# Performance work log

Hardware: AMD Instinct MI355X
Metric: run time of the kernel (lower is better)

## Reference

```python
import jax, jax.numpy as jnp
import numpy as np

K_NEIGHBOURS = 40  # includes self; self is dropped after top-k


def setup_inputs() -> dict:
    key = jax.random.key(0)
    ks = jax.random.split(key, 4)
    B, V, F_in = 4, 4096, 64
    P, S, F_out = 64, 4, 64
    x = jax.random.normal(ks[0], (B, V, F_in), dtype=jnp.float32)
    Wf = jax.random.normal(ks[1], (F_in, P), dtype=jnp.float32) / np.sqrt(F_in)
    bf = jnp.zeros((P,), dtype=jnp.float32)
    Ws = jax.random.normal(ks[2], (F_in, S), dtype=jnp.float32) / np.sqrt(F_in)
    bs = jnp.zeros((S,), dtype=jnp.float32)
    Wo = jax.random.normal(ks[3], (F_in + 2 * P, F_out), dtype=jnp.float32) / np.sqrt(F_in + 2 * P)
    bo = jnpp = jnp.zeros((F_out,), dtype=jnp.float32)
    return {"x": x, "Wf": Wf, "bf": bf, "Ws": Ws, "bs": bs, "Wo": Wo, "bo": bo}


def _euclidean_squared(c):
    # c: [B, V, S] -> [B, V, V] squared pairwise distances
    sq = jnp.sum(c * c, axis=-1)  # [B, V]
    d2 = sq[:, :, None] + sq[:, None, :] - 2.0 * jnp.einsum('bvs,bus->bvu', c, c)
    return d2


def reference(x, Wf, bf, Ws, bs, Wo, bo):
    # learned spatial coordinates and propagated features
    coords = x @ Ws + bs            # [B, V, S]
    feats = x @ Wf + bf             # [B, V, P]

    d2 = _euclidean_squared(coords)                 # [B, V, V]
    neg_vals, idx = jax.lax.top_k(-d2, K_NEIGHBOURS)  # closest first (self at 0)
    nbr_idx = idx[:, :, 1:]                         # [B, V, K-1]
    dist = -neg_vals[:, :, 1:]                      # [B, V, K-1] (>= 0)

    # gauss_of_lin(d * 10) = exp(-|10 d|)
    w = jnp.exp(-jnp.abs(dist * 10.0))              # [B, V, K-1]

    # gather neighbour features per batch: [B, V, K-1, P]
    nf = jax.vmap(lambda f, i: f[i])(feats, nbr_idx)
    nf = nf * w[..., None]

    collected = jnp.concatenate([jnp.max(nf, axis=2), jnp.mean(nf, axis=2)], axis=-1)  # [B, V, 2P]
    updated = jnp.concatenate([x, collected], axis=-1)  # [B, V, F_in + 2P]
    return jnp.tanh(updated @ Wo + bo)
```

## Files before the change

kernel.cpp:

```cpp
#include <hip/hip_runtime.h>
#include <cmath>

#define BB  4
#define VV  4096
#define KK  40
#define FIN 64

typedef float v2f __attribute__((ext_vector_type(2)));

__global__ __launch_bounds__(256) void prep_kernel(
    const float* __restrict__ x, const float* __restrict__ Wf,
    const float* __restrict__ bf, const float* __restrict__ Ws,
    const float* __restrict__ bs,
    float* __restrict__ coords, float* __restrict__ sq,
    float* __restrict__ feats)
{
    int lane = threadIdx.x & 63;
    int wid  = threadIdx.x >> 6;
    int row0 = (blockIdx.x * 4 + wid) * 4;
    const float* xr = x + (size_t)row0 * FIN;

    float rx0 = xr[lane];
    float rx1 = xr[64  + lane];
    float rx2 = xr[128 + lane];
    float rx3 = xr[192 + lane];

    float a0 = 0.f, a1 = 0.f, a2 = 0.f, a3 = 0.f;
    #pragma unroll
    for (int k = 0; k < FIN; ++k) {
        float wf = Wf[k * 64 + lane];
        a0 = fmaf(__uint_as_float(
             __builtin_amdgcn_readlane(__float_as_uint(rx0), k)), wf, a0);
        a1 = fmaf(__uint_as_float(
             __builtin_amdgcn_readlane(__float_as_uint(rx1), k)), wf, a1);
        a2 = fmaf(__uint_as_float(
             __builtin_amdgcn_readlane(__float_as_uint(rx2), k)), wf, a2);
        a3 = fmaf(__uint_as_float(
             __builtin_amdgcn_readlane(__float_as_uint(rx3), k)), wf, a3);
    }
    float bfl = bf[lane];
    feats[(size_t)(row0 + 0) * 64 + lane] = a0 + bfl;
    feats[(size_t)(row0 + 1) * 64 + lane] = a1 + bfl;
    feats[(size_t)(row0 + 2) * 64 + lane] = a2 + bfl;
    feats[(size_t)(row0 + 3) * 64 + lane] = a3 + bfl;

    int r  = lane >> 4;
    int s  = (lane >> 2) & 3;
    int kc = lane & 3;
    const float* xrr = x + (size_t)(row0 + r) * FIN + kc * 16;
    const float* wsr = Ws + kc * 16 * 4 + s;
    float c = 0.f;
    #pragma unroll
    for (int k = 0; k < 16; ++k)
        c = fmaf(xrr[k], wsr[k * 4], c);
    c += __shfl_xor(c, 1, 64);
    c += __shfl_xor(c, 2, 64);
    float val = c + bs[s];
    if ((lane & 3) == 0) coords[(size_t)(row0 + r) * 4 + s] = val;
    float p = val * val;
    p += __shfl_xor(p, 4, 64);
    p += __shfl_xor(p, 8, 64);
    if ((lane & 15) == 0) sq[row0 + r] = p;
}

__device__ __forceinline__ unsigned umed3(unsigned a, unsigned b, unsigned c)
{
    unsigned d;
    asm("v_med3_u32 %0, %1, %2, %3" : "=v"(d) : "v"(a), "v"(b), "v"(c));
    return d;
}

__device__ __forceinline__ unsigned bfi_key(unsigned maskv, unsigned d2b,
                                            unsigned u)
{
    unsigned d;
    asm("v_bfi_b32 %0, %1, %2, %3" : "=v"(d) : "v"(maskv), "v"(d2b), "v"(u));
    return d;
}

__device__ __forceinline__ int cnt_lt4(unsigned m0, unsigned m1,
                                       unsigned m2, unsigned m3,
                                       unsigned cand)
{
    return (int)__popcll(__ballot(m0 < cand))
         + (int)__popcll(__ballot(m1 < cand))
         + (int)__popcll(__ballot(m2 < cand))
         + (int)__popcll(__ballot(m3 < cand));
}

__device__ __forceinline__ unsigned select_thresh(unsigned m0, unsigned m1,
                                                  unsigned m2, unsigned m3)
{
    unsigned M = 0u;
    #pragma unroll
    for (int bit = 30; bit >= 12; --bit) {
        unsigned cand = M | (1u << bit);
        if (cnt_lt4(m0, m1, m2, m3, cand) <= 39) M = cand;
    }
    unsigned Msel = M | 0xFFFu;
    if (cnt_lt4(m0, m1, m2, m3, M + 4096u) != 40) {
        #pragma unroll
        for (int bit = 11; bit >= 0; --bit) {
            unsigned cand = M | (1u << bit);
            if (cnt_lt4(m0, m1, m2, m3, cand) <= 39) M = cand;
        }
        Msel = M;
    }
    return Msel;
}

__device__ __forceinline__ void compact4(unsigned m0, unsigned m1,
                                         unsigned m2, unsigned m3,
                                         unsigned Msel, uint2* dst)
{
    unsigned mn = m0;
    #pragma unroll
    for (int off = 32; off >= 1; off >>= 1) {
        unsigned o = __shfl_xor(mn, off, 64);
        mn = o < mn ? o : mn;
    }
    int base = 0;
    unsigned kk = m0;
    #pragma unroll
    for (int i = 0; i < 4; ++i) {
        bool pred = (kk <= Msel) && (kk != mn);
        unsigned long long mask = __ballot(pred);
        unsigned pos = (unsigned)base +
            __builtin_amdgcn_mbcnt_hi((unsigned)(mask >> 32),
                __builtin_amdgcn_mbcnt_lo((unsigned)mask, 0u));
        if (pred) {
            float d2a = __uint_as_float(kk & 0xFFFFF000u);
            float w   = __expf(-10.f * d2a);
            dst[pos] = make_uint2((kk & 4095u) << 8, __float_as_uint(w));
        }
        base += (int)__popcll(mask);
        kk = (i == 0) ? m1 : (i == 1) ? m2 : m3;
    }
}

__global__ __launch_bounds__(256, 8) void gravnet_kernel(
    const float* __restrict__ x, const float* __restrict__ coords,
    const float* __restrict__ sq, const float* __restrict__ feats,
    const float* __restrict__ Wo, const float* __restrict__ bo,
    float* __restrict__ out)
{
    int lane = threadIdx.x & 63;
    int w    = threadIdx.x >> 6;
    int quad = w >> 1;
    int half = w & 1;
    int bid  = (int)((blockIdx.x & 7) * 256 + (blockIdx.x >> 3));
    int qb   = bid * 8 + quad * 4;
    int b    = (bid * 8) >> 12;
    int v0   = qb & (VV - 1);

    __shared__ __align__(16) char smem[8192];
    uint4* s_mrg = (uint4*)smem;
    uint2* s_nb  = (uint2*)(smem + w * 2048);
    float* s_upd = (float*)(smem + w * 2048);

    const float4* cb  = (const float4*)(coords + (size_t)b * VV * 4);
    const float*  sqb = sq + (size_t)b * VV;

    float4 cq0 = cb[v0],     cq1 = cb[v0 + 1];
    float4 cq2 = cb[v0 + 2], cq3 = cb[v0 + 3];
    v2f nxA = (v2f){-2.f * cq0.x, -2.f * cq1.x};
    v2f nyA = (v2f){-2.f * cq0.y, -2.f * cq1.y};
    v2f nzA = (v2f){-2.f * cq0.z, -2.f * cq1.z};
    v2f nwA = (v2f){-2.f * cq0.w, -2.f * cq1.w};
    v2f hsA = (v2f){sqb[v0], sqb[v0 + 1]};
    v2f nxB = (v2f){-2.f * cq2.x, -2.f * cq3.x};
    v2f nyB = (v2f){-2.f * cq2.y, -2.f * cq3.y};
    v2f nzB = (v2f){-2.f * cq2.z, -2.f * cq3.z};
    v2f nwB = (v2f){-2.f * cq2.w, -2.f * cq3.w};
    v2f hsB = (v2f){sqb[v0 + 2], sqb[v0 + 3]};

    unsigned k00 = ~0u, k01 = ~0u, k02 = ~0u, k03 = ~0u;
    unsigned k10 = ~0u, k11 = ~0u, k12 = ~0u, k13 = ~0u;
    unsigned k20 = ~0u, k21 = ~0u, k22 = ~0u, k23 = ~0u;
    unsigned k30 = ~0u, k31 = ~0u, k32 = ~0u, k33 = ~0u;

    unsigned maskv = 0xFFFFF000u;

    int i0 = half * 32;
    #pragma unroll 4
    for (int i = i0; i < i0 + 32; ++i) {
        int u = i * 64 + lane;
        float4 cu = cb[u];
        float squ = sqb[u];
        v2f accA = hsA + (v2f){squ, squ};
        accA = __builtin_elementwise_fma(nxA, (v2f){cu.x, cu.x}, accA);
        accA = __builtin_elementwise_fma(nyA, (v2f){cu.y, cu.y}, accA);
        accA = __builtin_elementwise_fma(nzA, (v2f){cu.z, cu.z}, accA);
        accA = __builtin_elementwise_fma(nwA, (v2f){cu.w, cu.w}, accA);
        v2f accB = hsB + (v2f){squ, squ};
        accB = __builtin_elementwise_fma(nxB, (v2f){cu.x, cu.x}, accB);
        accB = __builtin_elementwise_fma(nyB, (v2f){cu.y, cu.y}, accB);
        accB = __builtin_elementwise_fma(nzB, (v2f){cu.z, cu.z}, accB);
        accB = __builtin_elementwise_fma(nwB, (v2f){cu.w, cu.w}, accB);

        {
            float d2 = fmaxf(accA.x, 0.f);
            unsigned k = bfi_key(maskv, __float_as_uint(d2), (unsigned)u);
            unsigned n1 = umed3(k00, k01, k);
            unsigned n2 = umed3(k01, k02, k);
            unsigned n3 = umed3(k02, k03, k);
            k00 = min(k00, k); k01 = n1; k02 = n2; k03 = n3;
        }
        {
            float d2 = fmaxf(accA.y, 0.f);
            unsigned k = bfi_key(maskv, __float_as_uint(d2), (unsigned)u);
            unsigned n1 = umed3(k10, k11, k);
            unsigned n2 = umed3(k11, k12, k);
            unsigned n3 = umed3(k12, k13, k);
            k10 = min(k10, k); k11 = n1; k12 = n2; k13 = n3;
        }
        {
            float d2 = fmaxf(accB.x, 0.f);
            unsigned k = bfi_key(maskv, __float_as_uint(d2), (unsigned)u);
            unsigned n1 = umed3(k20, k21, k);
            unsigned n2 = umed3(k21, k22, k);
            unsigned n3 = umed3(k22, k23, k);
            k20 = min(k20, k); k21 = n1; k22 = n2; k23 = n3;
        }
        {
            float d2 = fmaxf(accB.y, 0.f);
            unsigned k = bfi_key(maskv, __float_as_uint(d2), (unsigned)u);
            unsigned n1 = umed3(k30, k31, k);
            unsigned n2 = umed3(k31, k32, k);
            unsigned n3 = umed3(k32, k33, k);
            k30 = min(k30, k); k31 = n1; k32 = n2; k33 = n3;
        }
    }

    uint4 pub0 = half ? make_uint4(k00, k01, k02, k03)
                      : make_uint4(k20, k21, k22, k23);
    uint4 pub1 = half ? make_uint4(k10, k11, k12, k13)
                      : make_uint4(k30, k31, k32, k33);
    s_mrg[(w * 2 + 0) * 64 + lane] = pub0;
    s_mrg[(w * 2 + 1) * 64 + lane] = pub1;
    __syncthreads();

    int p   = w ^ 1;
    int lq0 = half * 2;
    uint4 pb0 = s_mrg[(p * 2 + 0) * 64 + lane];
    uint4 pb1 = s_mrg[(p * 2 + 1) * 64 + lane];
    unsigned oa0 = half ? k20 : k00, oa1 = half ? k21 : k01;
    unsigned oa2 = half ? k22 : k02, oa3 = half ? k23 : k03;
    unsigned ob0 = half ? k30 : k10, ob1 = half ? k31 : k11;
    unsigned ob2 = half ? k32 : k12, ob3 = half ? k33 : k13;
    __syncthreads();

    unsigned d0 = min(oa0, pb0.w), d1 = min(oa1, pb0.z);
    unsigned d2 = min(oa2, pb0.y), d3 = min(oa3, pb0.x);
    unsigned A0 = min(d0, d3), A3 = max(d0, d3);
    unsigned e0 = min(ob0, pb1.w), e1 = min(ob1, pb1.z);
    unsigned e2 = min(ob2, pb1.y), e3 = min(ob3, pb1.x);
    unsigned B0 = min(e0, e3), B3 = max(e0, e3);

    compact4(A0, d1, d2, A3, select_thresh(A0, d1, d2, A3), &s_nb[0]);
    compact4(B0, e1, e2, B3, select_thresh(B0, e1, e2, B3), &s_nb[KK]);

    const float* fb  = feats + (size_t)b * VV * 64;
    const char*  fbl = (const char*)(fb + lane);
    v2f vmax01 = (v2f){-INFINITY, -INFINITY};
    v2f vsum01 = (v2f){0.f, 0.f};
    #pragma unroll 6
    for (int j = 0; j < KK - 1; ++j) {
        uint2 n0 = s_nb[j];
        uint2 n1 = s_nb[KK + j];
        float f0 = *(const float*)(fbl + n0.x);
        float f1 = *(const float*)(fbl + n1.x);
        v2f g01 = (v2f){f0, f1} *
                  (v2f){__uint_as_float(n0.y), __uint_as_float(n1.y)};
        vmax01 = __builtin_elementwise_max(vmax01, g01);
        vsum01 += g01;
    }

    int q0g = qb + lq0, q1g = qb + lq0 + 1;
    float* sb = s_upd;
    *(float2*)&sb[lane * 2] =
        make_float2(x[(size_t)q0g * 64 + lane], x[(size_t)q1g * 64 + lane]);
    *(float2*)&sb[128 + lane * 2] = make_float2(vmax01.x, vmax01.y);
    *(float2*)&sb[256 + lane * 2] =
        make_float2(vsum01.x * (1.0f / 39.0f), vsum01.y * (1.0f / 39.0f));

    float bol = bo[lane];
    v2f acc01 = (v2f){bol, bol};
    #pragma unroll 8
    for (int jj = 0; jj < 96; ++jj) {
        float wo0 = Wo[(jj * 2 + 0) * 64 + lane];
        float wo1 = Wo[(jj * 2 + 1) * 64 + lane];
        float4 up = *(const float4*)&sb[jj * 4];
        acc01 = __builtin_elementwise_fma((v2f){up.x, up.y},
                                          (v2f){wo0, wo0}, acc01);
        acc01 = __builtin_elementwise_fma((v2f){up.z, up.w},
                                          (v2f){wo1, wo1}, acc01);
    }
    float e0t = __expf(2.f * acc01.x);
    float e1t = __expf(2.f * acc01.y);
    out[(size_t)q0g * 64 + lane] = 1.f - __fdividef(2.f, e0t + 1.f);
    out[(size_t)q1g * 64 + lane] = 1.f - __fdividef(2.f, e1t + 1.f);
}

extern "C" void kernel_launch(void* const* d_in, const int* in_sizes, int n_in,
                              void* d_out, int out_size, void* d_ws, size_t ws_size,
                              hipStream_t stream)
{
    (void)in_sizes; (void)n_in; (void)out_size; (void)ws_size;
    const float* x  = (const float*)d_in[0];
    const float* Wf = (const float*)d_in[1];
    const float* bf = (const float*)d_in[2];
    const float* Ws = (const float*)d_in[3];
    const float* bs = (const float*)d_in[4];
    const float* Wo = (const float*)d_in[5];
    const float* bo = (const float*)d_in[6];
    float* out = (float*)d_out;

    float* coords = (float*)d_ws;
    float* sq     = coords + (size_t)BB * VV * 4;
    float* feats  = sq + (size_t)BB * VV;

    prep_kernel<<<BB * VV / 16, 256, 0, stream>>>(x, Wf, bf, Ws, bs,
                                                  coords, sq, feats);
    gravnet_kernel<<<BB * VV / 8, 256, 0, stream>>>(x, coords, sq, feats,
                                                    Wo, bo, out);
}
```

Baseline: 118.9 us.

## Precompute x@Wo partial product in prep kernel and skip it in main kernel

Moves the x-part of the output projection (x times the first 64 rows of Wo) into the prep kernel, reusing the readlane-broadcast x values already used for feats, and stores it to a workspace buffer X2. A new main kernel variant seeds its accumulator from X2 and only multiplies the 128 collected features by the remaining Wo rows. This shortens the tail matmul of the latency-heavy main kernel, at the cost of extra FMAs in prep plus writing and re-reading a B*V*64 buffer. It falls back to the old kernel if the workspace is too small.

```diff
diff --git a/kernel.cpp b/kernel.cpp
--- a/kernel.cpp
+++ b/kernel.cpp
@@ -11,9 +11,9 @@
 __global__ __launch_bounds__(256) void prep_kernel(
     const float* __restrict__ x, const float* __restrict__ Wf,
     const float* __restrict__ bf, const float* __restrict__ Ws,
-    const float* __restrict__ bs,
+    const float* __restrict__ bs, const float* __restrict__ Wo,
     float* __restrict__ coords, float* __restrict__ sq,
-    float* __restrict__ feats)
+    float* __restrict__ feats, float* __restrict__ X2)
 {
     int lane = threadIdx.x & 63;
     int wid  = threadIdx.x >> 6;
@@ -26,23 +26,42 @@
     float rx3 = xr[192 + lane];
 
     float a0 = 0.f, a1 = 0.f, a2 = 0.f, a3 = 0.f;
+    float y0 = 0.f, y1 = 0.f, y2 = 0.f, y3 = 0.f;
+    bool do_x2 = (X2 != nullptr);
     #pragma unroll
     for (int k = 0; k < FIN; ++k) {
         float wf = Wf[k * 64 + lane];
-        a0 = fmaf(__uint_as_float(
-             __builtin_amdgcn_readlane(__float_as_uint(rx0), k)), wf, a0);
-        a1 = fmaf(__uint_as_float(
-             __builtin_amdgcn_readlane(__float_as_uint(rx1), k)), wf, a1);
-        a2 = fmaf(__uint_as_float(
-             __builtin_amdgcn_readlane(__float_as_uint(rx2), k)), wf, a2);
-        a3 = fmaf(__uint_as_float(
-             __builtin_amdgcn_readlane(__float_as_uint(rx3), k)), wf, a3);
+        float s0 = __uint_as_float(
+             __builtin_amdgcn_readlane(__float_as_uint(rx0), k));
+        float s1 = __uint_as_float(
+             __builtin_amdgcn_readlane(__float_as_uint(rx1), k));
+        float s2 = __uint_as_float(
+             __builtin_amdgcn_readlane(__float_as_uint(rx2), k));
+        float s3 = __uint_as_float(
+             __builtin_amdgcn_readlane(__float_as_uint(rx3), k));
+        a0 = fmaf(s0, wf, a0);
+        a1 = fmaf(s1, wf, a1);
+        a2 = fmaf(s2, wf, a2);
+        a3 = fmaf(s3, wf, a3);
+        if (do_x2) {
+            float wo = Wo[k * 64 + lane];
+            y0 = fmaf(s0, wo, y0);
+            y1 = fmaf(s1, wo, y1);
+            y2 = fmaf(s2, wo, y2);
+            y3 = fmaf(s3, wo, y3);
+        }
     }
     float bfl = bf[lane];
     feats[(size_t)(row0 + 0) * 64 + lane] = a0 + bfl;
     feats[(size_t)(row0 + 1) * 64 + lane] = a1 + bfl;
     feats[(size_t)(row0 + 2) * 64 + lane] = a2 + bfl;
     feats[(size_t)(row0 + 3) * 64 + lane] = a3 + bfl;
+    if (do_x2) {
+        X2[(size_t)(row0 + 0) * 64 + lane] = y0;
+        X2[(size_t)(row0 + 1) * 64 + lane] = y1;
+        X2[(size_t)(row0 + 2) * 64 + lane] = y2;
+        X2[(size_t)(row0 + 3) * 64 + lane] = y3;
+    }
 
     int r  = lane >> 4;
     int s  = (lane >> 2) & 3;
@@ -138,6 +157,187 @@
     }
 }
 
+__global__ __launch_bounds__(256, 8) void gravnet_x2(
+    const float* __restrict__ coords, const float* __restrict__ sq,
+    const float* __restrict__ feats, const float* __restrict__ Wo,
+    const float* __restrict__ bo, const float* __restrict__ X2,
+    float* __restrict__ out)
+{
+    int lane = threadIdx.x & 63;
+    int w    = threadIdx.x >> 6;
+    int quad = w >> 1;
+    int half = w & 1;
+    int bid  = (int)((blockIdx.x & 7) * 256 + (blockIdx.x >> 3));
+    int qb   = bid * 8 + quad * 4;
+    int b    = (bid * 8) >> 12;
+    int v0   = qb & (VV - 1);
+
+    __shared__ __align__(16) char smem[8192];
+    uint4* s_mrg = (uint4*)smem;
+    uint2* s_nb  = (uint2*)(smem + w * 2048);
+    float* s_upd = (float*)(smem + w * 2048);
+
+    const float4* cb  = (const float4*)(coords + (size_t)b * VV * 4);
+    const float*  sqb = sq + (size_t)b * VV;
+
+    float4 cq0 = cb[v0],     cq1 = cb[v0 + 1];
+    float4 cq2 = cb[v0 + 2], cq3 = cb[v0 + 3];
+    v2f nxA = (v2f){-2.f * cq0.x, -2.f * cq1.x};
+    v2f nyA = (v2f){-2.f * cq0.y, -2.f * cq1.y};
+    v2f nzA = (v2f){-2.f * cq0.z, -2.f * cq1.z};
+    v2f nwA = (v2f){-2.f * cq0.w, -2.f * cq1.w};
+    v2f hsA = (v2f){sqb[v0], sqb[v0 + 1]};
+    v2f nxB = (v2f){-2.f * cq2.x, -2.f * cq3.x};
+    v2f nyB = (v2f){-2.f * cq2.y, -2.f * cq3.y};
+    v2f nzB = (v2f){-2.f * cq2.z, -2.f * cq3.z};
+    v2f nwB = (v2f){-2.f * cq2.w, -2.f * cq3.w};
+    v2f hsB = (v2f){sqb[v0 + 2], sqb[v0 + 3]};
+
+    unsigned k00 = ~0u, k01 = ~0u, k02 = ~0u, k03 = ~0u;
+    unsigned k10 = ~0u, k11 = ~0u, k12 = ~0u, k13 = ~0u;
+    unsigned k20 = ~0u, k21 = ~0u, k22 = ~0u, k23 = ~0u;
+    unsigned k30 = ~0u, k31 = ~0u, k32 = ~0u, k33 = ~0u;
+
+    unsigned maskv = 0xFFFFF000u;
+
+    int i0 = half * 32;
+    #pragma unroll 8
+    for (int i = i0; i < i0 + 32; ++i) {
+        int u = i * 64 + lane;
+        float4 cu = cb[u];
+        float squ = sqb[u];
+        v2f accA = hsA + (v2f){squ, squ};
+        accA = __builtin_elementwise_fma(nxA, (v2f){cu.x, cu.x}, accA);
+        accA = __builtin_elementwise_fma(nyA, (v2f){cu.y, cu.y}, accA);
+        accA = __builtin_elementwise_fma(nzA, (v2f){cu.z, cu.z}, accA);
+        accA = __builtin_elementwise_fma(nwA, (v2f){cu.w, cu.w}, accA);
+        v2f accB = hsB + (v2f){squ, squ};
+        accB = __builtin_elementwise_fma(nxB, (v2f){cu.x, cu.x}, accB);
+        accB = __builtin_elementwise_fma(nyB, (v2f){cu.y, cu.y}, accB);
+        accB = __builtin_elementwise_fma(nzB, (v2f){cu.z, cu.z}, accB);
+        accB = __builtin_elementwise_fma(nwB, (v2f){cu.w, cu.w}, accB);
+
+        {
+            float d2 = fmaxf(accA.x, 0.f);
+            unsigned k = bfi_key(maskv, __float_as_uint(d2), (unsigned)u);
+            unsigned n1 = umed3(k00, k01, k);
+            unsigned n2 = umed3(k01, k02, k);
+            unsigned n3 = umed3(k02, k03, k);
+            k00 = min(k00, k); k01 = n1; k02 = n2; k03 = n3;
+        }
+        {
+            float d2 = fmaxf(accA.y, 0.f);
+            unsigned k = bfi_key(maskv, __float_as_uint(d2), (unsigned)u);
+            unsigned n1 = umed3(k10, k11, k);
+            unsigned n2 = umed3(k11, k12, k);
+            unsigned n3 = umed3(k12, k13, k);
+            k10 = min(k10, k); k11 = n1; k12 = n2; k13 = n3;
+        }
+        {
+            float d2 = fmaxf(accB.x, 0.f);
+            unsigned k = bfi_key(maskv, __float_as_uint(d2), (unsigned)u);
+            unsigned n1 = umed3(k20, k21, k);
+            unsigned n2 = umed3(k21, k22, k);
+            unsigned n3 = umed3(k22, k23, k);
+            k20 = min(k20, k); k21 = n1; k22 = n2; k23 = n3;
+        }
+        {
+            float d2 = fmaxf(accB.y, 0.f);
+            unsigned k = bfi_key(maskv, __float_as_uint(d2), (unsigned)u);
+            unsigned n1 = umed3(k30, k31, k);
+            unsigned n2 = umed3(k31, k32, k);
+            unsigned n3 = umed3(k32, k33, k);
+            k30 = min(k30, k); k31 = n1; k32 = n2; k33 = n3;
+        }
+    }
+
+    uint4 pub0 = half ? make_uint4(k00, k01, k02, k03)
+                      : make_uint4(k20, k21, k22, k23);
+    uint4 pub1 = half ? make_uint4(k10, k11, k12, k13)
+                      : make_uint4(k30, k31, k32, k33);
+    s_mrg[(w * 2 + 0) * 64 + lane] = pub0;
+    s_mrg[(w * 2 + 1) * 64 + lane] = pub1;
+    __syncthreads();
+
+    int p   = w ^ 1;
+    int lq0 = half * 2;
+    uint4 pb0 = s_mrg[(p * 2 + 0) * 64 + lane];
+    uint4 pb1 = s_mrg[(p * 2 + 1) * 64 + lane];
+    unsigned oa0 = half ? k20 : k00, oa1 = half ? k21 : k01;
+    unsigned oa2 = half ? k22 : k02, oa3 = half ? k23 : k03;
+    unsigned ob0 = half ? k30 : k10, ob1 = half ? k31 : k11;
+    unsigned ob2 = half ? k32 : k12, ob3 = half ? k33 : k13;
+    __syncthreads();
+
+    unsigned d0 = min(oa0, pb0.w), d1 = min(oa1, pb0.z);
+    unsigned d2 = min(oa2, pb0.y), d3 = min(oa3, pb0.x);
+    unsigned A0 = min(d0, d3), A3 = max(d0, d3);
+    unsigned e0 = min(ob0, pb1.w), e1 = min(ob1, pb1.z);
+    unsigned e2 = min(ob2, pb1.y), e3 = min(ob3, pb1.x);
+    unsigned B0 = min(e0, e3), B3 = max(e0, e3);
+
+    compact4(A0, d1, d2, A3, select_thresh(A0, d1, d2, A3), &s_nb[0]);
+    compact4(B0, e1, e2, B3, select_thresh(B0, e1, e2, B3), &s_nb[KK]);
+
+    const float* fb  = feats + (size_t)b * VV * 64;
+    const char*  fbl = (const char*)(fb + lane);
+    const uint4* nb0 = (const uint4*)&s_nb[0];
+    const uint4* nb1 = (const uint4*)&s_nb[KK];
+    v2f vmax01 = (v2f){-INFINITY, -INFINITY};
+    v2f vsum01 = (v2f){0.f, 0.f};
+    #pragma unroll 4
+    for (int jp = 0; jp < 19; ++jp) {
+        uint4 a = nb0[jp];
+        uint4 c = nb1[jp];
+        float f0a = *(const float*)(fbl + a.x);
+        float f1a = *(const float*)(fbl + c.x);
+        float f0b = *(const float*)(fbl + a.z);
+        float f1b = *(const float*)(fbl + c.z);
+        v2f ga = (v2f){f0a, f1a} *
+                 (v2f){__uint_as_float(a.y), __uint_as_float(c.y)};
+        v2f gb = (v2f){f0b, f1b} *
+                 (v2f){__uint_as_float(a.w), __uint_as_float(c.w)};
+        vmax01 = __builtin_elementwise_max(vmax01,
+                 __builtin_elementwise_max(ga, gb));
+        vsum01 += ga + gb;
+    }
+    {
+        uint2 n0 = s_nb[38];
+        uint2 n1 = s_nb[KK + 38];
+        float f0 = *(const float*)(fbl + n0.x);
+        float f1 = *(const float*)(fbl + n1.x);
+        v2f g01 = (v2f){f0, f1} *
+                  (v2f){__uint_as_float(n0.y), __uint_as_float(n1.y)};
+        vmax01 = __builtin_elementwise_max(vmax01, g01);
+        vsum01 += g01;
+    }
+
+    int q0g = qb + lq0, q1g = qb + lq0 + 1;
+    float* sb = s_upd;
+    *(float2*)&sb[lane * 2] = make_float2(vmax01.x, vmax01.y);
+    *(float2*)&sb[128 + lane * 2] =
+        make_float2(vsum01.x * (1.0f / 39.0f), vsum01.y * (1.0f / 39.0f));
+
+    float bol = bo[lane];
+    v2f acc01 = (v2f){bol + X2[(size_t)q0g * 64 + lane],
+                      bol + X2[(size_t)q1g * 64 + lane]};
+    const float* woB = Wo + 64 * 64;
+    #pragma unroll 8
+    for (int jj = 0; jj < 64; ++jj) {
+        float wo0 = woB[(jj * 2 + 0) * 64 + lane];
+        float wo1 = woB[(jj * 2 + 1) * 64 + lane];
+        float4 up = *(const float4*)&sb[jj * 4];
+        acc01 = __builtin_elementwise_fma((v2f){up.x, up.y},
+                                          (v2f){wo0, wo0}, acc01);
+        acc01 = __builtin_elementwise_fma((v2f){up.z, up.w},
+                                          (v2f){wo1, wo1}, acc01);
+    }
+    float e0t = __expf(2.f * acc01.x);
+    float e1t = __expf(2.f * acc01.y);
+    out[(size_t)q0g * 64 + lane] = 1.f - __fdividef(2.f, e0t + 1.f);
+    out[(size_t)q1g * 64 + lane] = 1.f - __fdividef(2.f, e1t + 1.f);
+}
+
 __global__ __launch_bounds__(256, 8) void gravnet_kernel(
     const float* __restrict__ x, const float* __restrict__ coords,
     const float* __restrict__ sq, const float* __restrict__ feats,
@@ -306,7 +506,7 @@
                               void* d_out, int out_size, void* d_ws, size_t ws_size,
                               hipStream_t stream)
 {
-    (void)in_sizes; (void)n_in; (void)out_size; (void)ws_size;
+    (void)in_sizes; (void)n_in; (void)out_size;
     const float* x  = (const float*)d_in[0];
     const float* Wf = (const float*)d_in[1];
     const float* bf = (const float*)d_in[2];
@@ -319,9 +519,18 @@
     float* coords = (float*)d_ws;
     float* sq     = coords + (size_t)BB * VV * 4;
     float* feats  = sq + (size_t)BB * VV;
-
-    prep_kernel<<<BB * VV / 16, 256, 0, stream>>>(x, Wf, bf, Ws, bs,
-                                                  coords, sq, feats);
-    gravnet_kernel<<<BB * VV / 8, 256, 0, stream>>>(x, coords, sq, feats,
-                                                    Wo, bo, out);
-}
+    float* X2     = feats + (size_t)BB * VV * 64;
+
+    size_t need = ((size_t)BB * VV * 4 + (size_t)BB * VV
+                 + (size_t)BB * VV * 64 * 2) * sizeof(float);
+    bool use_x2 = (ws_size >= need);
+
+    prep_kernel<<<BB * VV / 16, 256, 0, stream>>>(
+        x, Wf, bf, Ws, bs, Wo, coords, sq, feats, use_x2 ? X2 : nullptr);
+    if (use_x2)
+        gravnet_x2<<<BB * VV / 8, 256, 0, stream>>>(coords, sq, feats,
+                                                    Wo, bo, X2, out);
+    else
+        gravnet_kernel<<<BB * VV / 8, 256, 0, stream>>>(x, coords, sq, feats,
+                                                        Wo, bo, out);
+}
```

New measurement: 138.3 us. +16.3%, slower.

## Give each wave two full queries and drop the cross-wave top-k merge

Applied to the files above, without the earlier changes.

Each wavefront now scans all 4096 candidates for two query points. Previously two waves each scanned half the candidates for four queries and then merged their partial top-k lists through shared memory with barriers. The shared-memory merge and both __syncthreads are gone, and blocks shrink to 128 threads with twice as many launched. The neighbour gather loop now reads two neighbour entries per 16-byte LDS load. In exchange, each loaded candidate coordinate feeds only two queries instead of four, which doubles the coordinate loads per distance computed.

```diff
diff --git a/kernel.cpp b/kernel.cpp
--- a/kernel.cpp
+++ b/kernel.cpp
@@ -138,7 +138,7 @@
     }
 }
 
-__global__ __launch_bounds__(256, 8) void gravnet_kernel(
+__global__ __launch_bounds__(128, 8) void gravnet_kernel(
     const float* __restrict__ x, const float* __restrict__ coords,
     const float* __restrict__ sq, const float* __restrict__ feats,
     const float* __restrict__ Wo, const float* __restrict__ bo,
@@ -146,44 +146,33 @@
 {
     int lane = threadIdx.x & 63;
     int w    = threadIdx.x >> 6;
-    int quad = w >> 1;
-    int half = w & 1;
-    int bid  = (int)((blockIdx.x & 7) * 256 + (blockIdx.x >> 3));
-    int qb   = bid * 8 + quad * 4;
-    int b    = (bid * 8) >> 12;
+    int bid  = (int)((blockIdx.x & 7) * 512 + (blockIdx.x >> 3));
+    int gw   = bid * 2 + w;
+    int qb   = gw * 2;
+    int b    = qb >> 12;
     int v0   = qb & (VV - 1);
 
-    __shared__ __align__(16) char smem[8192];
-    uint4* s_mrg = (uint4*)smem;
+    __shared__ __align__(16) char smem[4096];
     uint2* s_nb  = (uint2*)(smem + w * 2048);
     float* s_upd = (float*)(smem + w * 2048);
 
     const float4* cb  = (const float4*)(coords + (size_t)b * VV * 4);
     const float*  sqb = sq + (size_t)b * VV;
 
-    float4 cq0 = cb[v0],     cq1 = cb[v0 + 1];
-    float4 cq2 = cb[v0 + 2], cq3 = cb[v0 + 3];
+    float4 cq0 = cb[v0], cq1 = cb[v0 + 1];
     v2f nxA = (v2f){-2.f * cq0.x, -2.f * cq1.x};
     v2f nyA = (v2f){-2.f * cq0.y, -2.f * cq1.y};
     v2f nzA = (v2f){-2.f * cq0.z, -2.f * cq1.z};
     v2f nwA = (v2f){-2.f * cq0.w, -2.f * cq1.w};
     v2f hsA = (v2f){sqb[v0], sqb[v0 + 1]};
-    v2f nxB = (v2f){-2.f * cq2.x, -2.f * cq3.x};
-    v2f nyB = (v2f){-2.f * cq2.y, -2.f * cq3.y};
-    v2f nzB = (v2f){-2.f * cq2.z, -2.f * cq3.z};
-    v2f nwB = (v2f){-2.f * cq2.w, -2.f * cq3.w};
-    v2f hsB = (v2f){sqb[v0 + 2], sqb[v0 + 3]};
 
     unsigned k00 = ~0u, k01 = ~0u, k02 = ~0u, k03 = ~0u;
     unsigned k10 = ~0u, k11 = ~0u, k12 = ~0u, k13 = ~0u;
-    unsigned k20 = ~0u, k21 = ~0u, k22 = ~0u, k23 = ~0u;
-    unsigned k30 = ~0u, k31 = ~0u, k32 = ~0u, k33 = ~0u;
 
     unsigned maskv = 0xFFFFF000u;
 
-    int i0 = half * 32;
-    #pragma unroll 4
-    for (int i = i0; i < i0 + 32; ++i) {
+    #pragma unroll 8
+    for (int i = 0; i < 64; ++i) {
         int u = i * 64 + lane;
         float4 cu = cb[u];
         float squ = sqb[u];
@@ -192,11 +181,6 @@
         accA = __builtin_elementwise_fma(nyA, (v2f){cu.y, cu.y}, accA);
         accA = __builtin_elementwise_fma(nzA, (v2f){cu.z, cu.z}, accA);
         accA = __builtin_elementwise_fma(nwA, (v2f){cu.w, cu.w}, accA);
-        v2f accB = hsB + (v2f){squ, squ};
-        accB = __builtin_elementwise_fma(nxB, (v2f){cu.x, cu.x}, accB);
-        accB = __builtin_elementwise_fma(nyB, (v2f){cu.y, cu.y}, accB);
-        accB = __builtin_elementwise_fma(nzB, (v2f){cu.z, cu.z}, accB);
-        accB = __builtin_elementwise_fma(nwB, (v2f){cu.w, cu.w}, accB);
 
         {
             float d2 = fmaxf(accA.x, 0.f);
@@ -214,60 +198,38 @@
             unsigned n3 = umed3(k12, k13, k);
             k10 = min(k10, k); k11 = n1; k12 = n2; k13 = n3;
         }
-        {
-            float d2 = fmaxf(accB.x, 0.f);
-            unsigned k = bfi_key(maskv, __float_as_uint(d2), (unsigned)u);
-            unsigned n1 = umed3(k20, k21, k);
-            unsigned n2 = umed3(k21, k22, k);
-            unsigned n3 = umed3(k22, k23, k);
-            k20 = min(k20, k); k21 = n1; k22 = n2; k23 = n3;
-        }
-        {
-            float d2 = fmaxf(accB.y, 0.f);
-            unsigned k = bfi_key(maskv, __float_as_uint(d2), (unsigned)u);
-            unsigned n1 = umed3(k30, k31, k);
-            unsigned n2 = umed3(k31, k32, k);
-            unsigned n3 = umed3(k32, k33, k);
-            k30 = min(k30, k); k31 = n1; k32 = n2; k33 = n3;
-        }
-    }
-
-    uint4 pub0 = half ? make_uint4(k00, k01, k02, k03)
-                      : make_uint4(k20, k21, k22, k23);
-    uint4 pub1 = half ? make_uint4(k10, k11, k12, k13)
-                      : make_uint4(k30, k31, k32, k33);
-    s_mrg[(w * 2 + 0) * 64 + lane] = pub0;
-    s_mrg[(w * 2 + 1) * 64 + lane] = pub1;
-    __syncthreads();
-
-    int p   = w ^ 1;
-    int lq0 = half * 2;
-    uint4 pb0 = s_mrg[(p * 2 + 0) * 64 + lane];
-    uint4 pb1 = s_mrg[(p * 2 + 1) * 64 + lane];
-    unsigned oa0 = half ? k20 : k00, oa1 = half ? k21 : k01;
-    unsigned oa2 = half ? k22 : k02, oa3 = half ? k23 : k03;
-    unsigned ob0 = half ? k30 : k10, ob1 = half ? k31 : k11;
-    unsigned ob2 = half ? k32 : k12, ob3 = half ? k33 : k13;
-    __syncthreads();
-
-    unsigned d0 = min(oa0, pb0.w), d1 = min(oa1, pb0.z);
-    unsigned d2 = min(oa2, pb0.y), d3 = min(oa3, pb0.x);
-    unsigned A0 = min(d0, d3), A3 = max(d0, d3);
-    unsigned e0 = min(ob0, pb1.w), e1 = min(ob1, pb1.z);
-    unsigned e2 = min(ob2, pb1.y), e3 = min(ob3, pb1.x);
-    unsigned B0 = min(e0, e3), B3 = max(e0, e3);
-
-    compact4(A0, d1, d2, A3, select_thresh(A0, d1, d2, A3), &s_nb[0]);
-    compact4(B0, e1, e2, B3, select_thresh(B0, e1, e2, B3), &s_nb[KK]);
+    }
+
+    compact4(k00, k01, k02, k03,
+             select_thresh(k00, k01, k02, k03), &s_nb[0]);
+    compact4(k10, k11, k12, k13,
+             select_thresh(k10, k11, k12, k13), &s_nb[KK]);
 
     const float* fb  = feats + (size_t)b * VV * 64;
     const char*  fbl = (const char*)(fb + lane);
+    const uint4* nb0 = (const uint4*)&s_nb[0];
+    const uint4* nb1 = (const uint4*)&s_nb[KK];
     v2f vmax01 = (v2f){-INFINITY, -INFINITY};
     v2f vsum01 = (v2f){0.f, 0.f};
-    #pragma unroll 6
-    for (int j = 0; j < KK - 1; ++j) {
-        uint2 n0 = s_nb[j];
-        uint2 n1 = s_nb[KK + j];
+    #pragma unroll 4
+    for (int jp = 0; jp < 19; ++jp) {
+        uint4 a = nb0[jp];
+        uint4 c = nb1[jp];
+        float f0a = *(const float*)(fbl + a.x);
+        float f1a = *(const float*)(fbl + c.x);
+        float f0b = *(const float*)(fbl + a.z);
+        float f1b = *(const float*)(fbl + c.z);
+        v2f ga = (v2f){f0a, f1a} *
+                 (v2f){__uint_as_float(a.y), __uint_as_float(c.y)};
+        v2f gb = (v2f){f0b, f1b} *
+                 (v2f){__uint_as_float(a.w), __uint_as_float(c.w)};
+        vmax01 = __builtin_elementwise_max(vmax01,
+                 __builtin_elementwise_max(ga, gb));
+        vsum01 += ga + gb;
+    }
+    {
+        uint2 n0 = s_nb[38];
+        uint2 n1 = s_nb[KK + 38];
         float f0 = *(const float*)(fbl + n0.x);
         float f1 = *(const float*)(fbl + n1.x);
         v2f g01 = (v2f){f0, f1} *
@@ -276,7 +238,7 @@
         vsum01 += g01;
     }
 
-    int q0g = qb + lq0, q1g = qb + lq0 + 1;
+    int q0g = qb, q1g = qb + 1;
     float* sb = s_upd;
     *(float2*)&sb[lane * 2] =
         make_float2(x[(size_t)q0g * 64 + lane], x[(size_t)q1g * 64 + lane]);
@@ -322,6 +284,6 @@
 
     prep_kernel<<<BB * VV / 16, 256, 0, stream>>>(x, Wf, bf, Ws, bs,
                                                   coords, sq, feats);
-    gravnet_kernel<<<BB * VV / 8, 256, 0, stream>>>(x, coords, sq, feats,
+    gravnet_kernel<<<BB * VV / 4, 128, 0, stream>>>(x, coords, sq, feats,
                                                     Wo, bo, out);
 }
```

New measurement: 126.9 us. 6.7% more time.
